# Performance work log

Hardware: AMD Instinct MI355X
Metric: run time of the kernel (lower is better)

## Reference

```python
import jax, jax.numpy as jnp
import numpy as np

HEADS, DIM_HEADS = 16, 16
SCALE = DIM_HEADS ** -0.5

# (forward_perm, inverse_perm) for each axial dim of x: (B, S, E, H, W)
# axial axes are 1 (seq), 3 (H=4), 4 (W=5); emb axis 2 moved to last, axial axis to second-last
_PERMS = [
    ((0, 3, 4, 1, 2), (0, 3, 4, 1, 2)),  # seq axis (self-inverse)
    ((0, 1, 4, 3, 2), (0, 1, 4, 3, 2)),  # H axis (self-inverse)
    ((0, 1, 3, 4, 2), (0, 1, 4, 2, 3)),  # W axis
]


def _self_attn(x, wq, wkv, wo_w, wo_b):
    # x: (..., t, d); standard multi-head self-attention along t
    q = x @ wq.T                               # (..., t, 256)
    k, v = jnp.split(x @ wkv.T, 2, axis=-1)    # each (..., t, 256)
    lead, tlen = x.shape[:-2], x.shape[-2]
    sh = (*lead, tlen, HEADS, DIM_HEADS)
    q, k, v = q.reshape(sh), k.reshape(sh), v.reshape(sh)
    scores = jnp.einsum('...thd,...shd->...hts', q, k) * SCALE
    attn = jax.nn.softmax(scores, axis=-1)
    o = jnp.einsum('...hts,...shd->...thd', attn, v)
    o = o.reshape(*lead, tlen, HEADS * DIM_HEADS)
    return o @ wo_w.T + wo_b


def _axial_attention_layer(x, wq_l, wkv_l, wo_w_l, wo_b_l):
    # sum of attention along each axial dim (sum_axial_out=True)
    out = jnp.zeros_like(x)
    for a, (p, ip) in enumerate(_PERMS):
        y = jnp.transpose(x, p)
        y = _self_attn(y, wq_l[a], wkv_l[a], wo_w_l[a], wo_b_l[a])
        out = out + jnp.transpose(y, ip)
    return out


def setup_inputs() -> dict:
    key = jax.random.key(0)
    ks = jax.random.split(key, 8)
    B, S, E, H, W = 32, 64, 256, 4, 5
    return {
        'x': jax.random.normal(ks[0], (B, S, E, H, W), jnp.float32),
        'pos_s': jax.random.normal(ks[1], (1, S, E, 1, 1), jnp.float32),
        'pos_h': jax.random.normal(ks[2], (1, 1, E, H, 1), jnp.float32),
        'pos_w': jax.random.normal(ks[3], (1, 1, E, 1, W), jnp.float32),
        'wq': jax.random.normal(ks[4], (2, 3, 256, E), jnp.float32) * 0.02,
        'wkv': jax.random.normal(ks[5], (2, 3, 512, E), jnp.float32) * 0.02,
        'wo_w': jax.random.normal(ks[6], (2, 3, E, 256), jnp.float32) * 0.02,
        'wo_b': jnp.zeros((2, 3, E), jnp.float32),
        'dec_w': jax.random.normal(ks[7], (1, E), jnp.float32) * 0.02,
        'dec_b': jnp.zeros((1,), jnp.float32),
    }


def reference(x, pos_s, pos_h, pos_w, wq, wkv, wo_w, wo_b, dec_w, dec_b):
    # additive axial positional embeddings
    x = x + pos_s + pos_h + pos_w
    # two stacked AxialAttention blocks (no residual in the wrapper)
    for l in range(2):
        x = _axial_attention_layer(x, wq[l], wkv[l], wo_w[l], wo_b[l])
    # (B, S, E, H, W) -> (B, S, H, W, E), linear decode to 1 channel, sigmoid
    x = jnp.transpose(x, (0, 1, 3, 4, 2))
    return jax.nn.sigmoid(x @ dec_w.T + dec_b)
```

## Files before the change

### kernel.cpp

```cpp
#include <hip/hip_runtime.h>
#include <stdint.h>

typedef unsigned short u16;
typedef u16 u16x8 __attribute__((ext_vector_type(8)));
typedef __bf16 bf16x8 __attribute__((ext_vector_type(8)));
typedef float f32x4 __attribute__((ext_vector_type(4)));
typedef float f32x16 __attribute__((ext_vector_type(16)));

#define NE   256
#define NPOS 40960
#define QLD  1536

__device__ __forceinline__ float bf2f(u16 h) {
  union { unsigned u; float f; } c; c.u = ((unsigned)h) << 16; return c.f;
}
__device__ __forceinline__ u16 f2bf(float f) {
  union { float f; unsigned u; } c; c.f = f;
  unsigned u = c.u;
  return (u16)((u + 0x7FFFu + ((u >> 16) & 1u)) >> 16);
}
__device__ __forceinline__ unsigned pkbf(float a, float b) {
  unsigned r;
  asm("v_cvt_pk_bf16_f32 %0, %1, %2" : "=v"(r) : "v"(a), "v"(b));
  return r;
}
__device__ __forceinline__ void gll16(const void* g, void* l) {
  __builtin_amdgcn_global_load_lds(
      (const __attribute__((address_space(1))) void*)g,
      (__attribute__((address_space(3))) void*)l, 16, 0, 0);
}

__global__ __launch_bounds__(256) void prep_kernel(
    const float* __restrict__ x, const float* __restrict__ pos_s,
    const float* __restrict__ pos_h, const float* __restrict__ pos_w,
    u16* __restrict__ xb)
{
  __shared__ float Ls[256 * 21];
  const int bs = blockIdx.x;
  const int s  = bs & 63;
  const int tid = threadIdx.x;
  const float* xp = x + (size_t)bs * 5120;
  for (int i = tid; i < 5120; i += 256) {
    int e = i / 20, hw = i % 20;
    int h = hw / 5, w = hw % 5;
    float v = xp[i] + pos_s[s * 256 + e] + pos_h[e * 4 + h] + pos_w[e * 5 + w];
    Ls[e * 21 + hw] = v;
  }
  __syncthreads();
  u16* op = xb + (size_t)bs * 20 * 256;
  for (int i = tid; i < 5120; i += 256) {
    int nl = i >> 8, e = i & 255;
    op[nl * 256 + e] = f2bf(Ls[e * 21 + nl]);
  }
}

__global__ __launch_bounds__(256) void pack_qkv(
    const float* __restrict__ wq, const float* __restrict__ wkv, u16* __restrict__ dst)
{
  int i = blockIdx.x * 256 + threadIdx.x;
  int la = i / (768 * 256);
  int rem = i - la * (768 * 256);
  int r = rem >> 8, c = rem & 255;
  float v = (r < 256) ? wq[(size_t)la * 65536 + r * 256 + c] * 0.25f
                      : wkv[(size_t)la * 131072 + (r - 256) * 256 + c];
  dst[i] = f2bf(v);
}

__global__ __launch_bounds__(256) void pack_wo(
    const float* __restrict__ wo, u16* __restrict__ dst)
{
  int i = blockIdx.x * 256 + threadIdx.x;
  int l = i / 196608;
  int rem = i - l * 196608;
  int out = rem / 768, k = rem % 768;
  int a = k >> 8, in = k & 255;
  dst[i] = f2bf(wo[(size_t)(((l * 3 + a) * 256) + out) * 256 + in]);
}

__global__ __launch_bounds__(256) void pack_bias(
    const float* __restrict__ wo_b, float* __restrict__ bsum)
{
  int i = blockIdx.x * 256 + threadIdx.x;
  if (i < 512) {
    int l = i >> 8, c = i & 255;
    bsum[i] = wo_b[(l * 3 + 0) * 256 + c] + wo_b[(l * 3 + 1) * 256 + c]
            + wo_b[(l * 3 + 2) * 256 + c];
  }
}

template<int MODE>
__global__ __launch_bounds__(256, 2) void gemm_bt(
    const u16* __restrict__ A, const u16* __restrict__ B,
    u16* __restrict__ Cb, const float* __restrict__ bias,
    const float* __restrict__ dw, float* __restrict__ logit,
    int K, int ldc)
{
  __shared__ alignas(16) u16 As[128 * 32];
  __shared__ alignas(16) u16 Bs[128 * 32];
  const int tid  = threadIdx.x;
  const int bm   = blockIdx.x, bn = blockIdx.y;
  const int lane = tid & 63, w = tid >> 6;
  const int wr   = (w >> 1) * 64, wc = (w & 1) * 64;
  const int r16  = lane & 15, khi = lane >> 4;

  f32x4 acc[4][4] = {};

  const u16* gA = A + (size_t)bm * 128 * K;
  const u16* gB = B + (size_t)bn * 128 * K;

  const int nkt = K >> 5;
  for (int kt = 0; kt < nkt; ++kt) {
    const u16* tA = gA + kt * 32;
    const u16* tB = gB + kt * 32;
    for (int i = tid; i < 512; i += 256) {
      int row = i >> 2, seg = (i & 3) << 3;
      gll16(tA + (size_t)row * K + seg, (char*)As + i * 16);
      gll16(tB + (size_t)row * K + seg, (char*)Bs + i * 16);
    }
    asm volatile("s_waitcnt vmcnt(0)" ::: "memory");
    __syncthreads();

    bf16x8 af[4], bfr[4];
    #pragma unroll
    for (int m = 0; m < 4; ++m)
      af[m] = *(const bf16x8*)(As + (wr + m * 16 + r16) * 32 + khi * 8);
    #pragma unroll
    for (int n = 0; n < 4; ++n)
      bfr[n] = *(const bf16x8*)(Bs + (wc + n * 16 + r16) * 32 + khi * 8);
    #pragma unroll
    for (int m = 0; m < 4; ++m)
      #pragma unroll
      for (int n = 0; n < 4; ++n)
        acc[m][n] = __builtin_amdgcn_mfma_f32_16x16x32_bf16(af[m], bfr[n], acc[m][n], 0, 0, 0);
    __syncthreads();
  }

  const int row0 = bm * 128 + wr + khi * 4;
  const int col0 = bn * 128 + wc + r16;

  if constexpr (MODE == 4) {
    float dwv[4], bvv[4];
    #pragma unroll
    for (int n = 0; n < 4; ++n) {
      int c = col0 + n * 16;
      dwv[n] = dw[c];
      bvv[n] = bias[c];
    }
    #pragma unroll
    for (int m = 0; m < 4; ++m) {
      #pragma unroll
      for (int j = 0; j < 4; ++j) {
        float p = 0.f;
        #pragma unroll
        for (int n = 0; n < 4; ++n) p += (acc[m][n][j] + bvv[n]) * dwv[n];
        p += __shfl_xor(p, 1);
        p += __shfl_xor(p, 2);
        p += __shfl_xor(p, 4);
        p += __shfl_xor(p, 8);
        if (r16 == 0) atomicAdd(&logit[row0 + m * 16 + j], p);
      }
    }
  } else {
    #pragma unroll
    for (int m = 0; m < 4; ++m) {
      #pragma unroll
      for (int n = 0; n < 4; ++n) {
        int c = col0 + n * 16;
        float bv = (MODE == 3) ? bias[c] : 0.f;
        #pragma unroll
        for (int j = 0; j < 4; ++j) {
          int r = row0 + m * 16 + j;
          Cb[(size_t)r * ldc + c] = f2bf(acc[m][n][j] + bv);
        }
      }
    }
  }
}

__global__ __launch_bounds__(256) void attn_seq_mfma(
    const u16* __restrict__ QKV, u16* __restrict__ Ob)
{
  const int w = threadIdx.x >> 6, lane = threadIdx.x & 63;
  const int wid = blockIdx.x * 4 + w;
  const int hd = wid & 15, g = wid >> 4;
  const int gb = g / 20, gr = g % 20;
  const int nbase = gb * 1280 + gr;
  const int lo = lane & 31, hi = lane >> 5;

  bf16x8 kf[2], qf[2];
  #pragma unroll
  for (int t = 0; t < 2; ++t) {
    size_t r = (size_t)(nbase + (lo + 32 * t) * 20) * QLD;
    kf[t] = *(const bf16x8*)(QKV + r + 256 + hd * 16 + hi * 8);
    qf[t] = *(const bf16x8*)(QKV + r +       hd * 16 + hi * 8);
  }
  union { u16 a[8]; bf16x8 v; } vt[4];
  #pragma unroll
  for (int c = 0; c < 4; ++c)
    #pragma unroll
    for (int j = 0; j < 8; ++j)
      vt[c].a[j] = QKV[(size_t)(nbase + (c * 16 + hi * 8 + j) * 20) * QLD
                       + 512 + hd * 16 + lo];

  f32x16 s00 = {}, s10 = {}, s01 = {}, s11 = {};
  s00 = __builtin_amdgcn_mfma_f32_32x32x16_bf16(kf[0], qf[0], s00, 0, 0, 0);
  s10 = __builtin_amdgcn_mfma_f32_32x32x16_bf16(kf[1], qf[0], s10, 0, 0, 0);
  s01 = __builtin_amdgcn_mfma_f32_32x32x16_bf16(kf[0], qf[1], s01, 0, 0, 0);
  s11 = __builtin_amdgcn_mfma_f32_32x32x16_bf16(kf[1], qf[1], s11, 0, 0, 0);

  auto run_qt = [&](f32x16 t0, f32x16 t1, int qt) {
    float m = -1e30f;
    #pragma unroll
    for (int r = 0; r < 16; ++r) { m = fmaxf(m, t0[r]); m = fmaxf(m, t1[r]); }
    m = fmaxf(m, __shfl_xor(m, 32));
    const float C = 1.4426950408889634f;
    float mc = m * C;
    float sum = 0.f;
    #pragma unroll
    for (int r = 0; r < 16; ++r) {
      float p0 = __builtin_amdgcn_exp2f(t0[r] * C - mc);
      float p1 = __builtin_amdgcn_exp2f(t1[r] * C - mc);
      t0[r] = p0; t1[r] = p1; sum += p0; sum += p1;
    }
    sum += __shfl_xor(sum, 32);
    float inv = __builtin_amdgcn_rcpf(sum);
    #pragma unroll
    for (int r = 0; r < 16; ++r) { t0[r] *= inv; t1[r] *= inv; }

    f32x16 oa = {};
    #pragma unroll
    for (int c = 0; c < 4; ++c) {
      const int rb = 8 * (c & 1);
      const f32x16& tt = (c < 2) ? t0 : t1;
      unsigned X0 = pkbf(tt[rb + 0], tt[rb + 1]);
      unsigned X1 = pkbf(tt[rb + 2], tt[rb + 3]);
      unsigned Y0 = pkbf(tt[rb + 4], tt[rb + 5]);
      unsigned Y1 = pkbf(tt[rb + 6], tt[rb + 7]);
      unsigned X0p = __shfl_xor((int)X0, 32), X1p = __shfl_xor((int)X1, 32);
      unsigned Y0p = __shfl_xor((int)Y0, 32), Y1p = __shfl_xor((int)Y1, 32);
      union { unsigned u[4]; bf16x8 v; } pf;
      pf.u[0] = hi ? Y0p : X0;
      pf.u[1] = hi ? Y1p : X1;
      pf.u[2] = hi ? Y0  : X0p;
      pf.u[3] = hi ? Y1  : X1p;
      oa = __builtin_amdgcn_mfma_f32_32x32x16_bf16(vt[c].v, pf.v, oa, 0, 0, 0);
    }
    unsigned P0 = pkbf(oa[0], oa[1]);
    unsigned P1 = pkbf(oa[2], oa[3]);
    unsigned P2 = pkbf(oa[4], oa[5]);
    unsigned P3 = pkbf(oa[6], oa[7]);
    unsigned sP0 = __shfl_xor((int)P0, 32), sP1 = __shfl_xor((int)P1, 32);
    unsigned sP2 = __shfl_xor((int)P2, 32), sP3 = __shfl_xor((int)P3, 32);
    union { unsigned u[4]; u16x8 v; } ov;
    ov.u[0] = hi ? sP2 : P0;
    ov.u[1] = hi ? sP3 : P1;
    ov.u[2] = hi ? P2  : sP0;
    ov.u[3] = hi ? P3  : sP1;
    u16* po = Ob + (size_t)(nbase + (qt * 32 + lo) * 20) * 768 + hd * 16 + hi * 8;
    *(u16x8*)po = ov.v;
  };
  run_qt(s00, s10, 0);
  run_qt(s01, s11, 1);
}

template<int T>
__device__ __forceinline__ void attn1(
    const u16* __restrict__ QKV, int n, int base, int stp, int hd,
    u16* __restrict__ po)
{
  const u16* qp = QKV + (size_t)n * QLD + hd * 16;
  u16x8 q0 = *(const u16x8*)(qp), q1 = *(const u16x8*)(qp + 8);
  float q[16];
  #pragma unroll
  for (int d = 0; d < 8; ++d) { q[d] = bf2f(q0[d]); q[d + 8] = bf2f(q1[d]); }

  float s[T];
  float m = -1e30f;
  #pragma unroll
  for (int j = 0; j < T; ++j) {
    const u16* kp = QKV + (size_t)(base + j * stp) * QLD + 256 + hd * 16;
    u16x8 k0 = *(const u16x8*)(kp), k1 = *(const u16x8*)(kp + 8);
    float a = 0.f;
    #pragma unroll
    for (int d = 0; d < 8; ++d) a += q[d] * bf2f(k0[d]) + q[d + 8] * bf2f(k1[d]);
    s[j] = a;
    m = fmaxf(m, a);
  }
  float sum = 0.f;
  float o[16];
  #pragma unroll
  for (int d = 0; d < 16; ++d) o[d] = 0.f;
  #pragma unroll
  for (int j = 0; j < T; ++j) {
    float pj = __expf(s[j] - m);
    sum += pj;
    const u16* vp = QKV + (size_t)(base + j * stp) * QLD + 512 + hd * 16;
    u16x8 w0 = *(const u16x8*)(vp), w1 = *(const u16x8*)(vp + 8);
    #pragma unroll
    for (int d = 0; d < 8; ++d) { o[d] += pj * bf2f(w0[d]); o[d + 8] += pj * bf2f(w1[d]); }
  }
  float inv = 1.0f / sum;
  u16x8 r0, r1;
  #pragma unroll
  for (int d = 0; d < 8; ++d) { r0[d] = f2bf(o[d] * inv); r1[d] = f2bf(o[d + 8] * inv); }
  *(u16x8*)(po)     = r0;
  *(u16x8*)(po + 8) = r1;
}

__global__ __launch_bounds__(256) void attn_hw(
    const u16* __restrict__ QKV, u16* __restrict__ Ob)
{
  const int tg = blockIdx.x * 256 + threadIdx.x;
  const int hd = tg & 15, n = tg >> 4;
  int h  = (n % 20) / 5;
  int w5 = n % 5;
  attn1<4>(QKV,       n, n - h * 5, 5, hd, Ob + (size_t)n * 768 + 256 + hd * 16);
  attn1<5>(QKV + 768, n, n - w5,    1, hd, Ob + (size_t)n * 768 + 512 + hd * 16);
}

__global__ __launch_bounds__(256) void sigmoid_kernel(
    const float* __restrict__ logit, const float* __restrict__ dec_b,
    float* __restrict__ out)
{
  int i = blockIdx.x * 256 + threadIdx.x;
  out[i] = 1.0f / (1.0f + __expf(-(logit[i] + dec_b[0])));
}

extern "C" void kernel_launch(void* const* d_in, const int* in_sizes, int n_in,
                              void* d_out, int out_size, void* d_ws, size_t ws_size,
                              hipStream_t stream) {
  const float* x     = (const float*)d_in[0];
  const float* pos_s = (const float*)d_in[1];
  const float* pos_h = (const float*)d_in[2];
  const float* pos_w = (const float*)d_in[3];
  const float* wq    = (const float*)d_in[4];
  const float* wkv   = (const float*)d_in[5];
  const float* wo_w  = (const float*)d_in[6];
  const float* wo_b  = (const float*)d_in[7];
  const float* dec_w = (const float*)d_in[8];
  const float* dec_b = (const float*)d_in[9];
  float* out = (float*)d_out;

  char* ws = (char*)d_ws;
  u16*   xb    = (u16*)ws;
  u16*   Ob    = (u16*)(ws + 20971520);
  u16*   QKV   = (u16*)(ws + 83886080);
  u16*   wqp   = (u16*)(ws + 209715200);
  u16*   wop   = (u16*)(ws + 212074496);
  float* bsum  = (float*)(ws + 212860928);
  float* logit = (float*)(ws + 212862976);

  prep_kernel<<<2048, 256, 0, stream>>>(x, pos_s, pos_h, pos_w, xb);
  pack_qkv<<<4608, 256, 0, stream>>>(wq, wkv, wqp);
  pack_wo<<<1536, 256, 0, stream>>>(wo_w, wop);
  pack_bias<<<2, 256, 0, stream>>>(wo_b, bsum);
  hipMemsetAsync(logit, 0, NPOS * sizeof(float), stream);

  for (int l = 0; l < 2; ++l) {
    gemm_bt<0><<<dim3(320, 6), 256, 0, stream>>>(
        xb, wqp + (size_t)(l * 3) * 196608, QKV, nullptr, nullptr, nullptr, 256, QLD);
    attn_seq_mfma<<<2560, 256, 0, stream>>>(QKV, Ob);
    gemm_bt<0><<<dim3(320, 12), 256, 0, stream>>>(
        xb, wqp + (size_t)(l * 3 + 1) * 196608, QKV, nullptr, nullptr, nullptr, 256, QLD);
    attn_hw<<<2560, 256, 0, stream>>>(QKV, Ob);
    if (l == 0)
      gemm_bt<3><<<dim3(320, 2), 256, 0, stream>>>(
          Ob, wop, xb, bsum, nullptr, nullptr, 768, 256);
    else
      gemm_bt<4><<<dim3(320, 2), 256, 0, stream>>>(
          Ob, wop + 196608, nullptr, bsum + 256, dec_w, logit, 768, 0);
  }

  sigmoid_kernel<<<NPOS / 256, 256, 0, stream>>>(logit, dec_b, out);
}
```

Baseline: 367.2 us.

## Double-buffer GEMM LDS tiles and widen N tile for QKV projections

After: 354.7 us. -3.4%, faster.

```diff
diff --git a/kernel.cpp b/kernel.cpp
--- a/kernel.cpp
+++ b/kernel.cpp
@@ -28,6 +28,11 @@
   __builtin_amdgcn_global_load_lds(
       (const __attribute__((address_space(1))) void*)g,
       (__attribute__((address_space(3))) void*)l, 16, 0, 0);
+}
+template<int N> __device__ __forceinline__ void waitvm() {
+  if constexpr (N == 0)      asm volatile("s_waitcnt vmcnt(0)" ::: "memory");
+  else if constexpr (N == 4) asm volatile("s_waitcnt vmcnt(4)" ::: "memory");
+  else if constexpr (N == 6) asm volatile("s_waitcnt vmcnt(6)" ::: "memory");
 }
 
 __global__ __launch_bounds__(256) void prep_kernel(
@@ -88,60 +93,82 @@
   }
 }
 
-template<int MODE>
+template<int MODE, int BN, int NKT>
 __global__ __launch_bounds__(256, 2) void gemm_bt(
     const u16* __restrict__ A, const u16* __restrict__ B,
     u16* __restrict__ Cb, const float* __restrict__ bias,
     const float* __restrict__ dw, float* __restrict__ logit,
-    int K, int ldc)
-{
-  __shared__ alignas(16) u16 As[128 * 32];
-  __shared__ alignas(16) u16 Bs[128 * 32];
+    int ldc)
+{
+  constexpr int K   = NKT * 32;
+  constexpr int NF  = BN / 32;
+  constexpr int LPT = 2 + BN / 64;
+  static_assert(MODE != 4 || BN == 128, "");
+
+  __shared__ alignas(16) u16 As[2][128 * 32];
+  __shared__ alignas(16) u16 Bs[2][BN * 32];
+
   const int tid  = threadIdx.x;
   const int bm   = blockIdx.x, bn = blockIdx.y;
   const int lane = tid & 63, w = tid >> 6;
-  const int wr   = (w >> 1) * 64, wc = (w & 1) * 64;
+  const int wr   = (w >> 1) * 64, wc = (w & 1) * (BN / 2);
   const int r16  = lane & 15, khi = lane >> 4;
 
-  f32x4 acc[4][4] = {};
+  f32x4 acc[4][NF] = {};
 
   const u16* gA = A + (size_t)bm * 128 * K;
-  const u16* gB = B + (size_t)bn * 128 * K;
-
-  const int nkt = K >> 5;
-  for (int kt = 0; kt < nkt; ++kt) {
+  const u16* gB = B + (size_t)bn * BN * K;
+
+  auto STAGE = [&](int kt, int which) {
     const u16* tA = gA + kt * 32;
     const u16* tB = gB + kt * 32;
-    for (int i = tid; i < 512; i += 256) {
+    #pragma unroll
+    for (int r = 0; r < 2; ++r) {
+      int i = tid + r * 256;
       int row = i >> 2, seg = (i & 3) << 3;
-      gll16(tA + (size_t)row * K + seg, (char*)As + i * 16);
-      gll16(tB + (size_t)row * K + seg, (char*)Bs + i * 16);
-    }
-    asm volatile("s_waitcnt vmcnt(0)" ::: "memory");
-    __syncthreads();
-
-    bf16x8 af[4], bfr[4];
+      gll16(tA + (size_t)row * K + seg, (char*)&As[which][0] + i * 16);
+    }
+    #pragma unroll
+    for (int r = 0; r < BN / 64; ++r) {
+      int i = tid + r * 256;
+      int row = i >> 2, seg = (i & 3) << 3;
+      gll16(tB + (size_t)row * K + seg, (char*)&Bs[which][0] + i * 16);
+    }
+  };
+
+  STAGE(0, 0);
+  #pragma unroll
+  for (int kt = 0; kt < NKT; ++kt) {
+    const int cur = kt & 1;
+    if (kt + 1 < NKT) { STAGE(kt + 1, cur ^ 1); waitvm<LPT>(); }
+    else              { waitvm<0>(); }
+    __builtin_amdgcn_s_barrier();
+    asm volatile("" ::: "memory");
+
+    bf16x8 af[4], bfr[NF];
     #pragma unroll
     for (int m = 0; m < 4; ++m)
-      af[m] = *(const bf16x8*)(As + (wr + m * 16 + r16) * 32 + khi * 8);
-    #pragma unroll
-    for (int n = 0; n < 4; ++n)
-      bfr[n] = *(const bf16x8*)(Bs + (wc + n * 16 + r16) * 32 + khi * 8);
+      af[m] = *(const bf16x8*)(&As[cur][0] + (wr + m * 16 + r16) * 32 + khi * 8);
+    #pragma unroll
+    for (int n = 0; n < NF; ++n)
+      bfr[n] = *(const bf16x8*)(&Bs[cur][0] + (wc + n * 16 + r16) * 32 + khi * 8);
     #pragma unroll
     for (int m = 0; m < 4; ++m)
       #pragma unroll
-      for (int n = 0; n < 4; ++n)
+      for (int n = 0; n < NF; ++n)
         acc[m][n] = __builtin_amdgcn_mfma_f32_16x16x32_bf16(af[m], bfr[n], acc[m][n], 0, 0, 0);
-    __syncthreads();
+
+    asm volatile("" ::: "memory");
+    __builtin_amdgcn_s_barrier();
   }
 
   const int row0 = bm * 128 + wr + khi * 4;
-  const int col0 = bn * 128 + wc + r16;
+  const int col0 = bn * BN + wc + r16;
 
   if constexpr (MODE == 4) {
-    float dwv[4], bvv[4];
-    #pragma unroll
-    for (int n = 0; n < 4; ++n) {
+    float dwv[NF], bvv[NF];
+    #pragma unroll
+    for (int n = 0; n < NF; ++n) {
       int c = col0 + n * 16;
       dwv[n] = dw[c];
       bvv[n] = bias[c];
@@ -152,7 +179,7 @@
       for (int j = 0; j < 4; ++j) {
         float p = 0.f;
         #pragma unroll
-        for (int n = 0; n < 4; ++n) p += (acc[m][n][j] + bvv[n]) * dwv[n];
+        for (int n = 0; n < NF; ++n) p += (acc[m][n][j] + bvv[n]) * dwv[n];
         p += __shfl_xor(p, 1);
         p += __shfl_xor(p, 2);
         p += __shfl_xor(p, 4);
@@ -164,7 +191,7 @@
     #pragma unroll
     for (int m = 0; m < 4; ++m) {
       #pragma unroll
-      for (int n = 0; n < 4; ++n) {
+      for (int n = 0; n < NF; ++n) {
         int c = col0 + n * 16;
         float bv = (MODE == 3) ? bias[c] : 0.f;
         #pragma unroll
@@ -357,18 +384,18 @@
   hipMemsetAsync(logit, 0, NPOS * sizeof(float), stream);
 
   for (int l = 0; l < 2; ++l) {
-    gemm_bt<0><<<dim3(320, 6), 256, 0, stream>>>(
-        xb, wqp + (size_t)(l * 3) * 196608, QKV, nullptr, nullptr, nullptr, 256, QLD);
+    gemm_bt<0, 256, 8><<<dim3(320, 3), 256, 0, stream>>>(
+        xb, wqp + (size_t)(l * 3) * 196608, QKV, nullptr, nullptr, nullptr, QLD);
     attn_seq_mfma<<<2560, 256, 0, stream>>>(QKV, Ob);
-    gemm_bt<0><<<dim3(320, 12), 256, 0, stream>>>(
-        xb, wqp + (size_t)(l * 3 + 1) * 196608, QKV, nullptr, nullptr, nullptr, 256, QLD);
+    gemm_bt<0, 256, 8><<<dim3(320, 6), 256, 0, stream>>>(
+        xb, wqp + (size_t)(l * 3 + 1) * 196608, QKV, nullptr, nullptr, nullptr, QLD);
     attn_hw<<<2560, 256, 0, stream>>>(QKV, Ob);
     if (l == 0)
-      gemm_bt<3><<<dim3(320, 2), 256, 0, stream>>>(
-          Ob, wop, xb, bsum, nullptr, nullptr, 768, 256);
+      gemm_bt<3, 128, 24><<<dim3(320, 2), 256, 0, stream>>>(
+          Ob, wop, xb, bsum, nullptr, nullptr, 256);
     else
-      gemm_bt<4><<<dim3(320, 2), 256, 0, stream>>>(
-          Ob, wop + 196608, nullptr, bsum + 256, dec_w, logit, 768, 0);
+      gemm_bt<4, 128, 24><<<dim3(320, 2), 256, 0, stream>>>(
+          Ob, wop + 196608, nullptr, bsum + 256, dec_w, logit, 0);
   }
 
   sigmoid_kernel<<<NPOS / 256, 256, 0, stream>>>(logit, dec_b, out);
```
